# Kernel optimization log

Measured on AMD Instinct MI355X. Metric: run time of the kernel, lower is better.

Reference implementation:

```python
import jax, jax.numpy as jnp
import numpy as np
from jax import lax

MAX_LEN = 40
SOS_ID = 2
VOCAB, EMB, HID, CTX = 32000, 512, 1024, 64
H2 = HID // 2
B, S = 256, 128


def gru_cell(x, h, wih, whh, bih, bhh):
    # PyTorch GRU equations: gates ordered (r, z, n)
    gx = x @ wih.T + bih
    gh = h @ whh.T + bhh
    rx, zx, nx = jnp.split(gx, 3, axis=-1)
    rh, zh, nh = jnp.split(gh, 3, axis=-1)
    r = jax.nn.sigmoid(rx + rh)
    z = jax.nn.sigmoid(zx + zh)
    n = jnp.tanh(nx + r * nh)
    return (1.0 - z) * n + z * h


def setup_inputs() -> dict:
    key = jax.random.key(0)
    ks = jax.random.split(key, 16)
    sd = 0.02
    emb_table = jax.random.normal(ks[0], (VOCAB, EMB), jnp.float32) * sd
    emb_table = emb_table.at[0].set(0.0)  # padding_idx=0
    def w(k, shape):
        return jax.random.normal(k, shape, jnp.float32) * sd
    inp = {
        "input_ids": jax.random.randint(ks[1], (B, S), 0, VOCAB),
        "context_vec": jax.random.normal(ks[2], (B, CTX), jnp.float32),
        "emb_table": emb_table,
        # encoder fwd direction
        "enc_wih_f": w(ks[3], (3 * H2, EMB)),
        "enc_whh_f": w(ks[4], (3 * H2, H2)),
        "enc_bih_f": w(ks[5], (3 * H2,)),
        "enc_bhh_f": w(ks[6], (3 * H2,)),
        # encoder bwd direction
        "enc_wih_b": w(ks[7], (3 * H2, EMB)),
        "enc_whh_b": w(ks[8], (3 * H2, H2)),
        "enc_bih_b": w(ks[9], (3 * H2,)),
        "enc_bhh_b": w(ks[10], (3 * H2,)),
        # decoder GRU: input = emb + hidden + context
        "dec_wih": w(ks[11], (3 * HID, EMB + HID + CTX)),
        "dec_whh": w(ks[12], (3 * HID, HID)),
        "dec_bih": w(ks[13], (3 * HID,)),
        "dec_bhh": w(ks[14], (3 * HID,)),
        "wout": w(ks[15], (VOCAB, HID)),
        "bout": jnp.zeros((VOCAB,), jnp.float32),
    }
    return inp


def reference(input_ids, context_vec, emb_table,
              enc_wih_f, enc_whh_f, enc_bih_f, enc_bhh_f,
              enc_wih_b, enc_whh_b, enc_bih_b, enc_bhh_b,
              dec_wih, dec_whh, dec_bih, dec_bhh, wout, bout):
    b = input_ids.shape[0]
    emb = emb_table[input_ids]                      # [B,S,E]
    emb_t = jnp.swapaxes(emb, 0, 1)                 # [S,B,E]

    def enc_f(h, x):
        return gru_cell(x, h, enc_wih_f, enc_whh_f, enc_bih_f, enc_bhh_f), None

    def enc_b(h, x):
        return gru_cell(x, h, enc_wih_b, enc_whh_b, enc_bih_b, enc_bhh_b), None

    h0 = jnp.zeros((b, H2), emb.dtype)
    hf, _ = lax.scan(enc_f, h0, emb_t)
    hb, _ = lax.scan(enc_b, h0, emb_t[::-1])
    # replicate torch's h_n.view(batch, -1) on a (2,B,H2) tensor (contiguous reshape)
    encoder_ctx = jnp.stack([hf, hb], axis=0).reshape(b, HID)   # [B,HID]

    ctx = jnp.concatenate([encoder_ctx, context_vec], axis=-1)  # [B,HID+CTX]
    h_dec0 = jnp.zeros((b, HID), emb.dtype)
    prev0 = jnp.full((b,), SOS_ID, dtype=jnp.int32)

    def dec_step(carry, _):
        h, prev = carry
        x = jnp.concatenate([emb_table[prev], ctx], axis=-1)
        h = gru_cell(x, h, dec_wih, dec_whh, dec_bih, dec_bhh)
        logits = h @ wout.T + bout                  # [B,V]
        probs = jax.nn.softmax(logits, axis=-1)
        nxt = jnp.argmax(probs, axis=-1).astype(jnp.int32)
        sel = jnp.take_along_axis(probs, nxt[:, None], axis=1)[:, 0]
        lp = jnp.log(sel + 1e-12)
        return (h, nxt), (nxt, lp)

    (_, _), (toks, lps) = lax.scan(dec_step, (h_dec0, prev0), None, length=MAX_LEN)
    return toks.T, lps.T   # [B,MAX_LEN] tokens, [B,MAX_LEN] log-probs
```

## Files before the change

### kernel.cpp

```cpp
#include <hip/hip_runtime.h>
#include <hip/hip_bf16.h>
#include <math.h>

#define B_    256
#define S_    128
#define EMB_  512
#define H2_   512
#define HID_  1024
#define CTX_  64
#define VOC_  32000
#define TMAX_ 40
#define SOS_  2

typedef unsigned short u16;
typedef __attribute__((ext_vector_type(8))) short short8;
typedef __attribute__((ext_vector_type(4))) float f32x4;

__device__ __forceinline__ float4 ld4(const float* p) {
    return *reinterpret_cast<const float4*>(p);
}
__device__ __forceinline__ float sigmoidf_(float x) { return 1.f / (1.f + expf(-x)); }
__device__ __forceinline__ u16 f2bf(float x) {
    union { float f; unsigned int u; } v; v.f = x;
    unsigned int r = v.u + 0x7FFFu + ((v.u >> 16) & 1u);
    return (u16)(r >> 16);
}
__device__ __forceinline__ unsigned pk2(float a, float b) {
    float2 t; t.x = a; t.y = b;
    __hip_bfloat162 h = __float22bfloat162_rn(t);
    return *reinterpret_cast<unsigned*>(&h);
}
__device__ __forceinline__ void merge_top2(float& v1, int& i1, float& v2, int& i2,
                                           float ov1, int oi1, float ov2, int oi2)
{
    if (ov1 > v1 || (ov1 == v1 && oi1 < i1)) {
        float tv = v1; int ti = i1;
        v1 = ov1; i1 = oi1;
        if (ov2 > tv || (ov2 == tv && oi2 < ti)) { v2 = ov2; i2 = oi2; }
        else                                     { v2 = tv;  i2 = ti;  }
    } else {
        if (ov1 > v2 || (ov1 == v2 && oi1 < i2)) { v2 = ov1; i2 = oi1; }
    }
}

template<int BM, int BN, int TM, int TN, int AMODE, int BGATHER, int BIASM>
__launch_bounds__(256)
__global__ void gemm_nt(const float* __restrict__ Ap,
                        const int*   __restrict__ ids,
                        const float* __restrict__ Ex,
                        const float* __restrict__ Bp, int ldb, int bofs,
                        const float* __restrict__ bias,
                        const float* __restrict__ addsrc,
                        float* __restrict__ Cp, int ldc,
                        int lda, int K, int s_base, int sdir)
{
    constexpr int BK = 32;
    __shared__ float As[BK][BM + 4];
    __shared__ float Bs[BK][BN + 4];
    const int t  = threadIdx.x;
    const int tx = t & 15, ty = t >> 4;
    const int m_base = blockIdx.y * BM;
    const int n_base = blockIdx.x * BN;

    float acc[TM][TN];
#pragma unroll
    for (int i = 0; i < TM; ++i)
#pragma unroll
        for (int j = 0; j < TN; ++j) acc[i][j] = 0.f;

    constexpr int A_PER = BM * BK / 4 / 256;
    constexpr int B_PER = BN * BK / 4 / 256;

    for (int k0 = 0; k0 < K; k0 += BK) {
#pragma unroll
        for (int j = 0; j < A_PER; ++j) {
            int f   = t + j * 256;
            int row = f >> 3;
            int kk  = (f & 7) << 2;
            int m   = m_base + row;
            float4 v;
            if constexpr (AMODE == 0) {
                v = ld4(Ap + (size_t)m * lda + k0 + kk);
            } else if constexpr (AMODE == 3) {
                int id = ids[m];
                v = ld4(Ex + (size_t)id * EMB_ + k0 + kk);
            } else {
                int k = k0 + kk;
                if (k < HID_) v = ld4(Ap + (size_t)m * HID_ + k);
                else          v = ld4(Ex + (size_t)m * CTX_ + (k - HID_));
            }
            As[kk + 0][row] = v.x; As[kk + 1][row] = v.y;
            As[kk + 2][row] = v.z; As[kk + 3][row] = v.w;
        }
#pragma unroll
        for (int j = 0; j < B_PER; ++j) {
            int f   = t + j * 256;
            int row = f >> 3;
            int kk  = (f & 7) << 2;
            float4 v;
            if constexpr (BGATHER == 1) {
                int n = n_base + row;
                int s = n >> 8, b = n & 255;
                int id = ids[b * S_ + s_base + sdir * s];
                v = ld4(Ex + (size_t)id * EMB_ + k0 + kk);
            } else {
                v = ld4(Bp + (size_t)(n_base + row) * ldb + bofs + k0 + kk);
            }
            Bs[kk + 0][row] = v.x; Bs[kk + 1][row] = v.y;
            Bs[kk + 2][row] = v.z; Bs[kk + 3][row] = v.w;
        }
        __syncthreads();
#pragma unroll
        for (int kk = 0; kk < BK; ++kk) {
            float a[TM], b[TN];
            *(float4*)&a[0] = ld4(&As[kk][ty * TM]);
            if constexpr (TM == 8) *(float4*)&a[4] = ld4(&As[kk][ty * TM + 4]);
            *(float4*)&b[0] = ld4(&Bs[kk][tx * TN]);
            if constexpr (TN == 8) *(float4*)&b[4] = ld4(&Bs[kk][tx * TN + 4]);
#pragma unroll
            for (int i = 0; i < TM; ++i)
#pragma unroll
                for (int j = 0; j < TN; ++j) acc[i][j] += a[i] * b[j];
        }
        __syncthreads();
    }
#pragma unroll
    for (int i = 0; i < TM; ++i) {
        int m = m_base + ty * TM + i;
#pragma unroll
        for (int j = 0; j < TN; ++j) {
            int n = n_base + tx * TN + j;
            float v = acc[i][j];
            if (bias) v += BIASM ? bias[m] : bias[n];
            if (addsrc) v += addsrc[(size_t)m * ldc + n];
            Cp[(size_t)m * ldc + n] = v;
        }
    }
}

__global__ void whh_trans(const float* __restrict__ whh_f, const float* __restrict__ whh_b,
                          float* __restrict__ whhX_f, float* __restrict__ whhX_b)
{
    int idx = blockIdx.x * 256 + threadIdx.x;
    const float* src = blockIdx.y ? whh_b : whh_f;
    float*       dst = blockIdx.y ? whhX_b : whhX_f;
    int k  = idx / 1536;
    int cc = idx - k * 1536;
    int u  = cc / 3;
    int g  = cc - u * 3;
    dst[idx] = src[(size_t)(g * 512 + u) * 512 + k];
}

#define RECBLK 128

union EncSM {
    struct { float hbuf[2][512][4]; float red[256][25]; } rec;
    struct { float As[32][132]; float Bs[32][132]; } gx;
};

__launch_bounds__(512)
__global__ void enc_fused(const float* __restrict__ grec_f, const float* __restrict__ grec_b,
                          float* __restrict__ gout_f, float* __restrict__ gout_b,
                          const float* __restrict__ whhX_f, const float* __restrict__ whhX_b,
                          const float* __restrict__ bhh_f, const float* __restrict__ bhh_b,
                          const float* __restrict__ wih_f, const float* __restrict__ wih_b,
                          const float* __restrict__ bih_f, const float* __restrict__ bih_b,
                          const int* __restrict__ ids, const float* __restrict__ emb,
                          float* __restrict__ hT, int do_rec, int gx_chunk, int nsteps)
{
    __shared__ __align__(16) EncSM sm;
    const int t = threadIdx.x;

    if (blockIdx.x >= RECBLK) {
        if (gx_chunk < 0) return;
        const int tt  = blockIdx.x - RECBLK;
        const int dz  = tt >= 192;
        const int t192 = dz ? tt - 192 : tt;
        const int m_base = (t192 & 15) * 128;
        const int n_base = (t192 >> 4) * 128;
        const float* W    = dz ? wih_b : wih_f;
        const float* bias = dz ? bih_b : bih_f;
        float*       Cp   = dz ? gout_b : gout_f;
        const int s_base  = dz ? (127 - 8 * gx_chunk) : (8 * gx_chunk);
        const int sdir    = dz ? -1 : 1;
        const int tx = t & 31, ty = t >> 5;

        float acc[8][4];
#pragma unroll
        for (int i = 0; i < 8; ++i)
#pragma unroll
            for (int j = 0; j < 4; ++j) acc[i][j] = 0.f;

        for (int k0 = 0; k0 < 512; k0 += 32) {
#pragma unroll
            for (int j = 0; j < 2; ++j) {
                int f   = t + j * 512;
                int row = f >> 3;
                int kk  = (f & 7) << 2;
                int m   = m_base + row;
                int s   = m >> 8, b = m & 255;
                int id  = ids[b * S_ + s_base + sdir * s];
                float4 v = ld4(emb + (size_t)id * EMB_ + k0 + kk);
                sm.gx.As[kk + 0][row] = v.x; sm.gx.As[kk + 1][row] = v.y;
                sm.gx.As[kk + 2][row] = v.z; sm.gx.As[kk + 3][row] = v.w;
                float4 wv = ld4(W + (size_t)(n_base + row) * 512 + k0 + kk);
                sm.gx.Bs[kk + 0][row] = wv.x; sm.gx.Bs[kk + 1][row] = wv.y;
                sm.gx.Bs[kk + 2][row] = wv.z; sm.gx.Bs[kk + 3][row] = wv.w;
            }
            __syncthreads();
#pragma unroll
            for (int kk = 0; kk < 32; ++kk) {
                float a[8], b[4];
                *(float4*)&a[0] = ld4(&sm.gx.As[kk][ty * 8]);
                *(float4*)&a[4] = ld4(&sm.gx.As[kk][ty * 8 + 4]);
                *(float4*)&b[0] = ld4(&sm.gx.Bs[kk][tx * 4]);
#pragma unroll
                for (int i = 0; i < 8; ++i)
#pragma unroll
                    for (int j = 0; j < 4; ++j) acc[i][j] += a[i] * b[j];
            }
            __syncthreads();
        }
#pragma unroll
        for (int i = 0; i < 8; ++i) {
            int m = m_base + ty * 8 + i;
#pragma unroll
            for (int j = 0; j < 4; ++j) {
                int n = n_base + tx * 4 + j;
                Cp[(size_t)m * 1536 + n] = acc[i][j] + bias[n];
            }
        }
        return;
    }

    if (!do_rec) return;
    const int bid = blockIdx.x;
    const int xcd = bid & 7;
    const int dir = xcd >> 2;
    const int local = (bid >> 3) * 4 + (xcd & 3);
    const int r0 = local * 4;
    const float* gx  = dir ? grec_b : grec_f;
    const float* whx = dir ? whhX_b : whhX_f;
    const float* bhh = dir ? bhh_b : bhh_f;
    float* hTd = hT + (size_t)dir * (256 * 512);

    const int kh = t >> 8;
    const int tu = t & 255;
    const int k_base = kh << 8;

    for (int i = t; i < 2048; i += 512) {
        int r = i >> 9, u = i & 511;
        sm.rec.hbuf[0][u][r] = hTd[(size_t)(r0 + r) * 512 + u];
    }
    float bh[2][3];
#pragma unroll
    for (int uu = 0; uu < 2; ++uu)
#pragma unroll
        for (int g = 0; g < 3; ++g)
            bh[uu][g] = bhh[g * 512 + tu * 2 + uu];
    __syncthreads();

    for (int st = 0; st < nsteps; ++st) {
        const int cur = st & 1, nxt = cur ^ 1;

        float2 gxv[3][4];
        if (!kh) {
#pragma unroll
            for (int g = 0; g < 3; ++g)
#pragma unroll
                for (int r = 0; r < 4; ++r)
                    gxv[g][r] = *(const float2*)&gx[(size_t)((st << 8) + r0 + r) * 1536
                                                    + (g << 9) + (tu << 1)];
        }

        float acc[2][3][4];
#pragma unroll
        for (int uu = 0; uu < 2; ++uu)
#pragma unroll
            for (int g = 0; g < 3; ++g)
#pragma unroll
                for (int r = 0; r < 4; ++r) acc[uu][g][r] = 0.f;

        const float* wp = whx + (size_t)k_base * 1536 + tu * 6;
#pragma unroll 4
        for (int kk = 0; kk < 256; ++kk) {
            float4 hv = *(const float4*)&sm.rec.hbuf[cur][k_base + kk][0];
            float2 w0 = *(const float2*)(wp + 0);
            float2 w1 = *(const float2*)(wp + 2);
            float2 w2 = *(const float2*)(wp + 4);
            const float* hvp = (const float*)&hv;
#pragma unroll
            for (int r = 0; r < 4; ++r) {
                float h = hvp[r];
                acc[0][0][r] += w0.x * h;
                acc[0][1][r] += w0.y * h;
                acc[0][2][r] += w1.x * h;
                acc[1][0][r] += w1.y * h;
                acc[1][1][r] += w2.x * h;
                acc[1][2][r] += w2.y * h;
            }
            wp += 1536;
        }

        if (kh) {
#pragma unroll
            for (int uu = 0; uu < 2; ++uu)
#pragma unroll
                for (int g = 0; g < 3; ++g)
#pragma unroll
                    for (int r = 0; r < 4; ++r)
                        sm.rec.red[tu][(uu * 3 + g) * 4 + r] = acc[uu][g][r];
        }
        __syncthreads();
        if (!kh) {
#pragma unroll
            for (int uu = 0; uu < 2; ++uu)
#pragma unroll
                for (int g = 0; g < 3; ++g)
#pragma unroll
                    for (int r = 0; r < 4; ++r)
                        acc[uu][g][r] += sm.rec.red[tu][(uu * 3 + g) * 4 + r];
#pragma unroll
            for (int uu = 0; uu < 2; ++uu) {
                int u = tu * 2 + uu;
#pragma unroll
                for (int r = 0; r < 4; ++r) {
                    float gr = uu ? gxv[0][r].y : gxv[0][r].x;
                    float gz = uu ? gxv[1][r].y : gxv[1][r].x;
                    float gn = uu ? gxv[2][r].y : gxv[2][r].x;
                    float hold = sm.rec.hbuf[cur][u][r];
                    float rg = sigmoidf_(gr + acc[uu][0][r] + bh[uu][0]);
                    float zg = sigmoidf_(gz + acc[uu][1][r] + bh[uu][1]);
                    float ng = tanhf(gn + rg * (acc[uu][2][r] + bh[uu][2]));
                    sm.rec.hbuf[nxt][u][r] = (1.f - zg) * ng + zg * hold;
                }
            }
        }
        __syncthreads();
    }

    const int lb = nsteps & 1;
    for (int i = t; i < 2048; i += 512) {
        int r = i >> 9, u = i & 511;
        hTd[(size_t)(r0 + r) * 512 + u] = sm.rec.hbuf[lb][u][r];
    }
}

__global__ void zerof(float* __restrict__ p, int n)
{
    int i = blockIdx.x * 256 + threadIdx.x;
    if (i < n) p[i] = 0.f;
}

__global__ void init_dec(float* __restrict__ hdec, u16* __restrict__ hbf, int* __restrict__ prev)
{
    int i = blockIdx.x * 256 + threadIdx.x;
    hdec[i] = 0.f; hbf[i] = 0;
    if (i < B_) prev[i] = SOS_;
}

__global__ void hcat_build(const float* __restrict__ hT, float* __restrict__ hcat)
{
    int idx = blockIdx.x * 256 + threadIdx.x;
    int b = idx >> 10, k = idx & 1023;
    int d = b >> 7;
    int rr = ((2 * b) & 255) + (k >> 9);
    int kk = k & 511;
    hcat[idx] = hT[(size_t)d * 131072 + (size_t)rr * 512 + kk];
}

__launch_bounds__(256)
__global__ void dec_gemm2(const float* __restrict__ hdec, const int* __restrict__ prev,
                          const float* __restrict__ emb,
                          const float* __restrict__ dwhh, const float* __restrict__ dwih,
                          const float* __restrict__ dbhh, const float* __restrict__ gctx,
                          float* __restrict__ ghbuf, float* __restrict__ gibuf)
{
    constexpr int BK = 32;
    __shared__ float As[BK][68];
    __shared__ float Bs[BK][68];
    const int t  = threadIdx.x;
    const int tx = t & 15, ty = t >> 4;
    const bool isH = blockIdx.y < 4;
    const int m_base = (isH ? blockIdx.y : (blockIdx.y - 4)) * 64;
    const int n_base = blockIdx.x * 64;
    const int K   = isH ? 1024 : 512;
    const float* Bp = isH ? dwhh : dwih;
    const int ldb  = isH ? 1024 : 1600;
    float* Cp = isH ? ghbuf : gibuf;

    float acc[4][4];
#pragma unroll
    for (int i = 0; i < 4; ++i)
#pragma unroll
        for (int j = 0; j < 4; ++j) acc[i][j] = 0.f;

    for (int k0 = 0; k0 < K; k0 += BK) {
#pragma unroll
        for (int j = 0; j < 2; ++j) {
            int f   = t + j * 256;
            int row = f >> 3;
            int kk  = (f & 7) << 2;
            int m   = m_base + row;
            float4 v;
            if (isH) v = ld4(hdec + (size_t)m * HID_ + k0 + kk);
            else     v = ld4(emb + (size_t)prev[m] * EMB_ + k0 + kk);
            As[kk + 0][row] = v.x; As[kk + 1][row] = v.y;
            As[kk + 2][row] = v.z; As[kk + 3][row] = v.w;
            float4 w = ld4(Bp + (size_t)(n_base + row) * ldb + k0 + kk);
            Bs[kk + 0][row] = w.x; Bs[kk + 1][row] = w.y;
            Bs[kk + 2][row] = w.z; Bs[kk + 3][row] = w.w;
        }
        __syncthreads();
#pragma unroll
        for (int kk = 0; kk < BK; ++kk) {
            float a[4], b[4];
            *(float4*)&a[0] = ld4(&As[kk][ty * 4]);
            *(float4*)&b[0] = ld4(&Bs[kk][tx * 4]);
#pragma unroll
            for (int i = 0; i < 4; ++i)
#pragma unroll
                for (int j = 0; j < 4; ++j) acc[i][j] += a[i] * b[j];
        }
        __syncthreads();
    }
#pragma unroll
    for (int i = 0; i < 4; ++i) {
        int m = m_base + ty * 4 + i;
#pragma unroll
        for (int j = 0; j < 4; ++j) {
            int n = n_base + tx * 4 + j;
            float v = acc[i][j];
            if (isH) v += dbhh[n];
            else     v += gctx[(size_t)m * 3072 + n];
            Cp[(size_t)m * 3072 + n] = v;
        }
    }
}

__global__ void dec_combine(const float* __restrict__ gi, const float* __restrict__ gh,
                            float* __restrict__ hdec, u16* __restrict__ hbf)
{
    int idx = blockIdx.x * 256 + threadIdx.x;
    int b = idx >> 10, u = idx & 1023;
    size_t gb = (size_t)b * 3072;
    float r = sigmoidf_(gi[gb + u]            + gh[gb + u]);
    float z = sigmoidf_(gi[gb + HID_ + u]     + gh[gb + HID_ + u]);
    float n = tanhf    (gi[gb + 2 * HID_ + u] + r * gh[gb + 2 * HID_ + u]);
    float v = (1.f - z) * n + z * hdec[idx];
    hdec[idx] = v;
    hbf[idx] = f2bf(v);
}

__launch_bounds__(512)
__global__ void gemm_logits(const u16* __restrict__ A, const float* __restrict__ Wf,
                            const float* __restrict__ bias,
                            float* __restrict__ pmax, float* __restrict__ psum,
                            float* __restrict__ ptv, int* __restrict__ pti)
{
    __shared__ u16 As[256][72];
    __shared__ u16 Bs[128][72];
    const int t = threadIdx.x;
    const int lane = t & 63, wave = t >> 6;
    const int wm = (wave & 3) * 64, wn = (wave >> 2) * 64;
    const int n0 = blockIdx.x * 128;
    f32x4 acc[4][4];
#pragma unroll
    for (int i = 0; i < 4; ++i)
#pragma unroll
        for (int j = 0; j < 4; ++j) acc[i][j] = (f32x4){0.f, 0.f, 0.f, 0.f};
    const int arow = t >> 1, aoff = (t & 1) * 32;
    const int brow = t >> 2, boff = (t & 3) * 16;

    for (int k0 = 0; k0 < 1024; k0 += 64) {
#pragma unroll
        for (int q = 0; q < 4; ++q) {
            *(uint4*)&As[arow][aoff + q * 8] =
                *(const uint4*)(A + (size_t)arow * 1024 + k0 + aoff + q * 8);
        }
        const float* wr = Wf + (size_t)(n0 + brow) * 1024 + k0 + boff;
#pragma unroll
        for (int q = 0; q < 2; ++q) {
            float4 x = ld4(wr + q * 8);
            float4 y = ld4(wr + q * 8 + 4);
            uint4 o;
            o.x = pk2(x.x, x.y); o.y = pk2(x.z, x.w);
            o.z = pk2(y.x, y.y); o.w = pk2(y.z, y.w);
            *(uint4*)&Bs[brow][boff + q * 8] = o;
        }
        __syncthreads();
#pragma unroll
        for (int s = 0; s < 2; ++s) {
            short8 a[4], b[4];
            int j0 = s * 32 + (lane >> 4) * 8;
#pragma unroll
            for (int i = 0; i < 4; ++i) {
                a[i] = *(const short8*)&As[wm + i * 16 + (lane & 15)][j0];
                b[i] = *(const short8*)&Bs[wn + i * 16 + (lane & 15)][j0];
            }
#pragma unroll
            for (int i = 0; i < 4; ++i)
#pragma unroll
                for (int j = 0; j < 4; ++j)
                    acc[i][j] = __builtin_amdgcn_mfma_f32_16x16x32_bf16(a[i], b[j], acc[i][j], 0, 0, 0);
        }
        __syncthreads();
    }

    const int htile = blockIdx.x * 2 + (wn >> 6);
    float bn[4]; int jx[4];
#pragma unroll
    for (int j = 0; j < 4; ++j) { jx[j] = n0 + wn + j * 16 + (lane & 15); bn[j] = bias[jx[j]]; }
#pragma unroll
    for (int i = 0; i < 4; ++i) {
#pragma unroll
        for (int rr = 0; rr < 4; ++rr) {
            float v[4];
#pragma unroll
            for (int j = 0; j < 4; ++j) v[j] = acc[i][j][rr] + bn[j];
            float v1 = v[0], v2 = -3.4e38f; int i1 = jx[0], i2 = 0x7fffffff;
#pragma unroll
            for (int j = 1; j < 4; ++j) {
                if (v[j] > v1)      { v2 = v1; i2 = i1; v1 = v[j]; i1 = jx[j]; }
                else if (v[j] > v2) { v2 = v[j]; i2 = jx[j]; }
            }
#pragma unroll
            for (int mask = 1; mask <= 8; mask <<= 1) {
                float ov1 = __shfl_xor(v1, mask), ov2 = __shfl_xor(v2, mask);
                int   oi1 = __shfl_xor(i1, mask), oi2 = __shfl_xor(i2, mask);
                merge_top2(v1, i1, v2, i2, ov1, oi1, ov2, oi2);
            }
            float rmax = v1;
            float s = 0.f;
#pragma unroll
            for (int j = 0; j < 4; ++j) s += expf(v[j] - rmax);
#pragma unroll
            for (int mask = 1; mask <= 8; mask <<= 1) s += __shfl_xor(s, mask);
            if ((lane & 15) == 0) {
                int row = wm + i * 16 + (lane >> 4) * 4 + rr;
                size_t base = (size_t)row * 500 + htile;
                pmax[base] = rmax; psum[base] = s;
                ptv[base * 2] = v1; ptv[base * 2 + 1] = v2;
                pti[base * 2] = i1; pti[base * 2 + 1] = i2;
            }
        }
    }
}

__launch_bounds__(256)
__global__ void dec_reduce(const float* __restrict__ pmax, const float* __restrict__ psum,
                           const float* __restrict__ ptv, const int* __restrict__ pti,
                           const float* __restrict__ hdec, const float* __restrict__ wout,
                           const float* __restrict__ bout,
                           float* __restrict__ out, int* __restrict__ prev, int tstep)
{
    __shared__ float sv[256]; __shared__ int sti[256]; __shared__ int ssl[256];
    __shared__ float cvv[1000]; __shared__ int cii[1000];
    __shared__ float c8v[8]; __shared__ int c8i[8]; __shared__ float c8e[8];
    const int b = blockIdx.x, tid = threadIdx.x;
    const float* pm = pmax + (size_t)b * 500;
    const float* ps = psum + (size_t)b * 500;

    float m = -3.4e38f;
    for (int i = tid; i < 500; i += 256) m = fmaxf(m, pm[i]);
    sv[tid] = m; __syncthreads();
    for (int off = 128; off; off >>= 1) { if (tid < off) sv[tid] = fmaxf(sv[tid], sv[tid + off]); __syncthreads(); }
    float gmax = sv[0]; __syncthreads();

    float s = 0.f;
    for (int i = tid; i < 500; i += 256) s += ps[i] * expf(pm[i] - gmax);
    sv[tid] = s; __syncthreads();
    for (int off = 128; off; off >>= 1) { if (tid < off) sv[tid] += sv[tid + off]; __syncthreads(); }
    float gsum = sv[0]; __syncthreads();

    for (int i = tid; i < 1000; i += 256) { cvv[i] = ptv[(size_t)b * 1000 + i]; cii[i] = pti[(size_t)b * 1000 + i]; }
    __syncthreads();

    for (int c = 0; c < 8; ++c) {
        float bv = -3.4e38f; int bi = 0x7fffffff, bs = 0;
        for (int i = tid; i < 1000; i += 256) {
            float v = cvv[i]; int ix = cii[i];
            if (v > bv || (v == bv && ix < bi)) { bv = v; bi = ix; bs = i; }
        }
        sv[tid] = bv; sti[tid] = bi; ssl[tid] = bs; __syncthreads();
        for (int off = 128; off; off >>= 1) {
            if (tid < off) {
                if (sv[tid + off] > sv[tid] ||
                    (sv[tid + off] == sv[tid] && sti[tid + off] < sti[tid])) {
                    sv[tid] = sv[tid + off]; sti[tid] = sti[tid + off]; ssl[tid] = ssl[tid + off];
                }
            }
            __syncthreads();
        }
        if (tid == 0) { c8v[c] = sv[0]; c8i[c] = sti[0]; cvv[ssl[0]] = -3.4e38f; }
        __syncthreads();
    }

    {
        int lane = tid & 63, wv = tid >> 6;
        const float* hr = hdec + (size_t)b * HID_;
        for (int c = wv; c < 8; c += 4) {
            const float* wr = wout + (size_t)c8i[c] * HID_;
            float a = 0.f;
            for (int k = lane * 4; k < HID_; k += 256) {
                float4 x = ld4(hr + k), y = ld4(wr + k);
                a += x.x * y.x + x.y * y.y + x.z * y.z + x.w * y.w;
            }
#pragma unroll
            for (int off = 32; off; off >>= 1) a += __shfl_down(a, off);
            if (lane == 0) c8e[c] = a + bout[c8i[c]];
        }
    }
    __syncthreads();

    if (tid == 0) {
        float bv = c8e[0]; int bi = c8i[0]; float av = c8v[0];
        for (int c = 1; c < 8; ++c)
            if (c8e[c] > bv || (c8e[c] == bv && c8i[c] < bi)) { bv = c8e[c]; bi = c8i[c]; av = c8v[c]; }
        float p = expf(av - gmax) / gsum;
        float lp = logf(p + 1e-12f);
        out[(size_t)b * TMAX_ + tstep] = (float)bi;
        out[B_ * TMAX_ + (size_t)b * TMAX_ + tstep] = lp;
        prev[b] = bi;
    }
}

extern "C" void kernel_launch(void* const* d_in, const int* in_sizes, int n_in,
                              void* d_out, int out_size, void* d_ws, size_t ws_size,
                              hipStream_t stream)
{
    const int*   ids   = (const int*)  d_in[0];
    const float* cvec  = (const float*)d_in[1];
    const float* emb   = (const float*)d_in[2];
    const float* wih_f = (const float*)d_in[3];
    const float* whh_f = (const float*)d_in[4];
    const float* bih_f = (const float*)d_in[5];
    const float* bhh_f = (const float*)d_in[6];
    const float* wih_b = (const float*)d_in[7];
    const float* whh_b = (const float*)d_in[8];
    const float* bih_b = (const float*)d_in[9];
    const float* bhh_b = (const float*)d_in[10];
    const float* dwih  = (const float*)d_in[11];
    const float* dwhh  = (const float*)d_in[12];
    const float* dbih  = (const float*)d_in[13];
    const float* dbhh  = (const float*)d_in[14];
    const float* wout  = (const float*)d_in[15];
    const float* bout  = (const float*)d_in[16];
    float* out = (float*)d_out;

    float* w      = (float*)d_ws;
    float* buf0_f = w;
    float* buf0_b = w + 3145728;
    float* buf1_f = w + 6291456;
    float* buf1_b = w + 9437184;
    float* hT     = w + 12582912;
    float* hcat   = w + 12845056;
    float* hdec   = w + 13107200;
    float* gctx   = w + 13369344;
    u16*   hdecb  = (u16*)(w + 14155776);
    int*   prev   = (int*)(w + 14286848);
    float* whhX_f = w + 14287104;
    float* whhX_b = w + 15073536;
    float* gibuf  = buf0_f;
    float* ghbuf  = buf0_f + 786432;
    float* pmax   = buf0_f + 1572864;
    float* psum   = buf0_f + 1700864;
    float* ptv    = buf0_f + 1828864;
    int*   pti    = (int*)(buf0_f + 2084864);

    zerof<<<1024, 256, 0, stream>>>(hT, 262144);
    init_dec<<<1024, 256, 0, stream>>>(hdec, hdecb, prev);
    whh_trans<<<dim3(3072, 2), 256, 0, stream>>>(whh_f, whh_b, whhX_f, whhX_b);

    enc_fused<<<512, 512, 0, stream>>>(
        buf0_f, buf0_b, buf0_f, buf0_b, whhX_f, whhX_b, bhh_f, bhh_b,
        wih_f, wih_b, bih_f, bih_b, ids, emb, hT, 0, 0, 8);
    for (int c = 1; c < 16; ++c) {
        float* rf = ((c - 1) & 1) ? buf1_f : buf0_f;
        float* rb = ((c - 1) & 1) ? buf1_b : buf0_b;
        float* of = (c & 1) ? buf1_f : buf0_f;
        float* ob = (c & 1) ? buf1_b : buf0_b;
        enc_fused<<<512, 512, 0, stream>>>(
            rf, rb, of, ob, whhX_f, whhX_b, bhh_f, bhh_b,
            wih_f, wih_b, bih_f, bih_b, ids, emb, hT, 1, c, 8);
    }
    enc_fused<<<512, 512, 0, stream>>>(
        buf1_f, buf1_b, buf1_f, buf1_b, whhX_f, whhX_b, bhh_f, bhh_b,
        wih_f, wih_b, bih_f, bih_b, ids, emb, hT, 1, -1, 8);

    hcat_build<<<1024, 256, 0, stream>>>(hT, hcat);

    gemm_nt<64, 64, 4, 4, 2, 0, 0><<<dim3(48, 4), 256, 0, stream>>>(
        hcat, nullptr, cvec, dwih, 1600, 512, dbih, nullptr,
        gctx, 3072, 1024, 1088, 0, 0);

    for (int t = 0; t < TMAX_; ++t) {
        dec_gemm2<<<dim3(48, 8), 256, 0, stream>>>(
            hdec, prev, emb, dwhh, dwih, dbhh, gctx, ghbuf, gibuf);
        dec_combine<<<1024, 256, 0, stream>>>(gibuf, ghbuf, hdec, hdecb);
        gemm_logits<<<dim3(250, 1), 512, 0, stream>>>(hdecb, wout, bout,
                                                      pmax, psum, ptv, pti);
        dec_reduce<<<256, 256, 0, stream>>>(pmax, psum, ptv, pti,
                                            hdec, wout, bout, out, prev, t);
    }
}
```

Before: 10.65 ms.

## Pre-convert output weights to bf16 and restructure encoder recurrence to one unit per thread

The encoder recurrent weights are now laid out gate-major (k, gate, unit), and each of the 512 threads computes one hidden unit over the full K=512. This removes the split-K shared-memory reduction and one barrier per step, at the cost of a longer serial dot product per thread. Separately, the 32000x1024 output projection is converted to bf16 once, so the per-step logits GEMM loads half the bytes and skips the repeated fp32-to-bf16 packing. That path is used only when the workspace is large enough, which adds one conversion kernel and about 64MB of scratch.

```diff
diff --git a/kernel.cpp b/kernel.cpp
--- a/kernel.cpp
+++ b/kernel.cpp
@@ -139,29 +139,36 @@
 }
 
 __global__ void whh_trans(const float* __restrict__ whh_f, const float* __restrict__ whh_b,
-                          float* __restrict__ whhX_f, float* __restrict__ whhX_b)
+                          float* __restrict__ whhU_f, float* __restrict__ whhU_b)
 {
     int idx = blockIdx.x * 256 + threadIdx.x;
     const float* src = blockIdx.y ? whh_b : whh_f;
-    float*       dst = blockIdx.y ? whhX_b : whhX_f;
+    float*       dst = blockIdx.y ? whhU_b : whhU_f;
     int k  = idx / 1536;
-    int cc = idx - k * 1536;
-    int u  = cc / 3;
-    int g  = cc - u * 3;
+    int rem = idx - k * 1536;
+    int g  = rem >> 9;
+    int u  = rem & 511;
     dst[idx] = src[(size_t)(g * 512 + u) * 512 + k];
 }
 
+__global__ void wbf_conv(const float* __restrict__ wout, unsigned* __restrict__ wbf)
+{
+    int idx = blockIdx.x * 256 + threadIdx.x;
+    float2 v = *reinterpret_cast<const float2*>(wout + (size_t)idx * 2);
+    wbf[idx] = pk2(v.x, v.y);
+}
+
 #define RECBLK 128
 
 union EncSM {
-    struct { float hbuf[2][512][4]; float red[256][25]; } rec;
+    struct { float hbuf[2][512][4]; } rec;
     struct { float As[32][132]; float Bs[32][132]; } gx;
 };
 
 __launch_bounds__(512)
 __global__ void enc_fused(const float* __restrict__ grec_f, const float* __restrict__ grec_b,
                           float* __restrict__ gout_f, float* __restrict__ gout_b,
-                          const float* __restrict__ whhX_f, const float* __restrict__ whhX_b,
+                          const float* __restrict__ whhU_f, const float* __restrict__ whhU_b,
                           const float* __restrict__ bhh_f, const float* __restrict__ bhh_b,
                           const float* __restrict__ wih_f, const float* __restrict__ wih_b,
                           const float* __restrict__ bih_f, const float* __restrict__ bih_b,
@@ -240,110 +247,63 @@
     const int local = (bid >> 3) * 4 + (xcd & 3);
     const int r0 = local * 4;
     const float* gx  = dir ? grec_b : grec_f;
-    const float* whx = dir ? whhX_b : whhX_f;
+    const float* whx = dir ? whhU_b : whhU_f;
     const float* bhh = dir ? bhh_b : bhh_f;
     float* hTd = hT + (size_t)dir * (256 * 512);
 
-    const int kh = t >> 8;
-    const int tu = t & 255;
-    const int k_base = kh << 8;
-
-    for (int i = t; i < 2048; i += 512) {
-        int r = i >> 9, u = i & 511;
+    const int u = t;
+
+#pragma unroll
+    for (int r = 0; r < 4; ++r)
         sm.rec.hbuf[0][u][r] = hTd[(size_t)(r0 + r) * 512 + u];
-    }
-    float bh[2][3];
-#pragma unroll
-    for (int uu = 0; uu < 2; ++uu)
-#pragma unroll
-        for (int g = 0; g < 3; ++g)
-            bh[uu][g] = bhh[g * 512 + tu * 2 + uu];
+    const float bh0 = bhh[u], bh1 = bhh[512 + u], bh2 = bhh[1024 + u];
     __syncthreads();
 
     for (int st = 0; st < nsteps; ++st) {
         const int cur = st & 1, nxt = cur ^ 1;
 
-        float2 gxv[3][4];
-        if (!kh) {
-#pragma unroll
-            for (int g = 0; g < 3; ++g)
-#pragma unroll
-                for (int r = 0; r < 4; ++r)
-                    gxv[g][r] = *(const float2*)&gx[(size_t)((st << 8) + r0 + r) * 1536
-                                                    + (g << 9) + (tu << 1)];
-        }
-
-        float acc[2][3][4];
-#pragma unroll
-        for (int uu = 0; uu < 2; ++uu)
-#pragma unroll
-            for (int g = 0; g < 3; ++g)
-#pragma unroll
-                for (int r = 0; r < 4; ++r) acc[uu][g][r] = 0.f;
-
-        const float* wp = whx + (size_t)k_base * 1536 + tu * 6;
-#pragma unroll 4
-        for (int kk = 0; kk < 256; ++kk) {
-            float4 hv = *(const float4*)&sm.rec.hbuf[cur][k_base + kk][0];
-            float2 w0 = *(const float2*)(wp + 0);
-            float2 w1 = *(const float2*)(wp + 2);
-            float2 w2 = *(const float2*)(wp + 4);
+        float gx0[4], gx1[4], gx2[4];
+#pragma unroll
+        for (int r = 0; r < 4; ++r) {
+            size_t base = (size_t)((st << 8) + r0 + r) * 1536 + u;
+            gx0[r] = gx[base];
+            gx1[r] = gx[base + 512];
+            gx2[r] = gx[base + 1024];
+        }
+
+        float acc0[4] = {0.f,0.f,0.f,0.f};
+        float acc1[4] = {0.f,0.f,0.f,0.f};
+        float acc2[4] = {0.f,0.f,0.f,0.f};
+        const float* wp = whx + u;
+#pragma unroll 8
+        for (int kk = 0; kk < 512; ++kk) {
+            float4 hv = *(const float4*)&sm.rec.hbuf[cur][kk][0];
+            float w0 = wp[0], w1 = wp[512], w2 = wp[1024];
             const float* hvp = (const float*)&hv;
 #pragma unroll
             for (int r = 0; r < 4; ++r) {
-                float h = hvp[r];
-                acc[0][0][r] += w0.x * h;
-                acc[0][1][r] += w0.y * h;
-                acc[0][2][r] += w1.x * h;
-                acc[1][0][r] += w1.y * h;
-                acc[1][1][r] += w2.x * h;
-                acc[1][2][r] += w2.y * h;
+                acc0[r] += w0 * hvp[r];
+                acc1[r] += w1 * hvp[r];
+                acc2[r] += w2 * hvp[r];
             }
             wp += 1536;
         }
 
-        if (kh) {
-#pragma unroll
-            for (int uu = 0; uu < 2; ++uu)
-#pragma unroll
-                for (int g = 0; g < 3; ++g)
-#pragma unroll
-                    for (int r = 0; r < 4; ++r)
-                        sm.rec.red[tu][(uu * 3 + g) * 4 + r] = acc[uu][g][r];
-        }
-        __syncthreads();
-        if (!kh) {
-#pragma unroll
-            for (int uu = 0; uu < 2; ++uu)
-#pragma unroll
-                for (int g = 0; g < 3; ++g)
-#pragma unroll
-                    for (int r = 0; r < 4; ++r)
-                        acc[uu][g][r] += sm.rec.red[tu][(uu * 3 + g) * 4 + r];
-#pragma unroll
-            for (int uu = 0; uu < 2; ++uu) {
-                int u = tu * 2 + uu;
-#pragma unroll
-                for (int r = 0; r < 4; ++r) {
-                    float gr = uu ? gxv[0][r].y : gxv[0][r].x;
-                    float gz = uu ? gxv[1][r].y : gxv[1][r].x;
-                    float gn = uu ? gxv[2][r].y : gxv[2][r].x;
-                    float hold = sm.rec.hbuf[cur][u][r];
-                    float rg = sigmoidf_(gr + acc[uu][0][r] + bh[uu][0]);
-                    float zg = sigmoidf_(gz + acc[uu][1][r] + bh[uu][1]);
-                    float ng = tanhf(gn + rg * (acc[uu][2][r] + bh[uu][2]));
-                    sm.rec.hbuf[nxt][u][r] = (1.f - zg) * ng + zg * hold;
-                }
-            }
+#pragma unroll
+        for (int r = 0; r < 4; ++r) {
+            float hold = sm.rec.hbuf[cur][u][r];
+            float rg = sigmoidf_(gx0[r] + acc0[r] + bh0);
+            float zg = sigmoidf_(gx1[r] + acc1[r] + bh1);
+            float ng = tanhf(gx2[r] + rg * (acc2[r] + bh2));
+            sm.rec.hbuf[nxt][u][r] = (1.f - zg) * ng + zg * hold;
         }
         __syncthreads();
     }
 
     const int lb = nsteps & 1;
-    for (int i = t; i < 2048; i += 512) {
-        int r = i >> 9, u = i & 511;
+#pragma unroll
+    for (int r = 0; r < 4; ++r)
         hTd[(size_t)(r0 + r) * 512 + u] = sm.rec.hbuf[lb][u][r];
-    }
 }
 
 __global__ void zerof(float* __restrict__ p, int n)
@@ -454,6 +414,7 @@
 
 __launch_bounds__(512)
 __global__ void gemm_logits(const u16* __restrict__ A, const float* __restrict__ Wf,
+                            const u16* __restrict__ Wbf,
                             const float* __restrict__ bias,
                             float* __restrict__ pmax, float* __restrict__ psum,
                             float* __restrict__ ptv, int* __restrict__ pti)
@@ -478,15 +439,21 @@
             *(uint4*)&As[arow][aoff + q * 8] =
                 *(const uint4*)(A + (size_t)arow * 1024 + k0 + aoff + q * 8);
         }
-        const float* wr = Wf + (size_t)(n0 + brow) * 1024 + k0 + boff;
-#pragma unroll
-        for (int q = 0; q < 2; ++q) {
-            float4 x = ld4(wr + q * 8);
-            float4 y = ld4(wr + q * 8 + 4);
-            uint4 o;
-            o.x = pk2(x.x, x.y); o.y = pk2(x.z, x.w);
-            o.z = pk2(y.x, y.y); o.w = pk2(y.z, y.w);
-            *(uint4*)&Bs[brow][boff + q * 8] = o;
+        if (Wbf) {
+            const u16* wr = Wbf + (size_t)(n0 + brow) * 1024 + k0 + boff;
+            *(uint4*)&Bs[brow][boff]     = *(const uint4*)(wr);
+            *(uint4*)&Bs[brow][boff + 8] = *(const uint4*)(wr + 8);
+        } else {
+            const float* wr = Wf + (size_t)(n0 + brow) * 1024 + k0 + boff;
+#pragma unroll
+            for (int q = 0; q < 2; ++q) {
+                float4 x = ld4(wr + q * 8);
+                float4 y = ld4(wr + q * 8 + 4);
+                uint4 o;
+                o.x = pk2(x.x, x.y); o.y = pk2(x.z, x.w);
+                o.z = pk2(y.x, y.y); o.w = pk2(y.z, y.w);
+                *(uint4*)&Bs[brow][boff + q * 8] = o;
+            }
         }
         __syncthreads();
 #pragma unroll
@@ -659,8 +626,10 @@
     float* gctx   = w + 13369344;
     u16*   hdecb  = (u16*)(w + 14155776);
     int*   prev   = (int*)(w + 14286848);
-    float* whhX_f = w + 14287104;
-    float* whhX_b = w + 15073536;
+    float* whhU_f = w + 14287104;
+    float* whhU_b = w + 15073536;
+    u16*   wbf    = (u16*)(w + 15859968);
+    const int use_wbf = (ws_size >= (size_t)(15859968 + 16384000) * 4);
     float* gibuf  = buf0_f;
     float* ghbuf  = buf0_f + 786432;
     float* pmax   = buf0_f + 1572864;
@@ -670,10 +639,10 @@
 
     zerof<<<1024, 256, 0, stream>>>(hT, 262144);
     init_dec<<<1024, 256, 0, stream>>>(hdec, hdecb, prev);
-    whh_trans<<<dim3(3072, 2), 256, 0, stream>>>(whh_f, whh_b, whhX_f, whhX_b);
+    whh_trans<<<dim3(3072, 2), 256, 0, stream>>>(whh_f, whh_b, whhU_f, whhU_b);
 
     enc_fused<<<512, 512, 0, stream>>>(
-        buf0_f, buf0_b, buf0_f, buf0_b, whhX_f, whhX_b, bhh_f, bhh_b,
+        buf0_f, buf0_b, buf0_f, buf0_b, whhU_f, whhU_b, bhh_f, bhh_b,
         wih_f, wih_b, bih_f, bih_b, ids, emb, hT, 0, 0, 8);
     for (int c = 1; c < 16; ++c) {
         float* rf = ((c - 1) & 1) ? buf1_f : buf0_f;
@@ -681,14 +650,17 @@
         float* of = (c & 1) ? buf1_f : buf0_f;
         float* ob = (c & 1) ? buf1_b : buf0_b;
         enc_fused<<<512, 512, 0, stream>>>(
-            rf, rb, of, ob, whhX_f, whhX_b, bhh_f, bhh_b,
+            rf, rb, of, ob, whhU_f, whhU_b, bhh_f, bhh_b,
             wih_f, wih_b, bih_f, bih_b, ids, emb, hT, 1, c, 8);
     }
     enc_fused<<<512, 512, 0, stream>>>(
-        buf1_f, buf1_b, buf1_f, buf1_b, whhX_f, whhX_b, bhh_f, bhh_b,
+        buf1_f, buf1_b, buf1_f, buf1_b, whhU_f, whhU_b, bhh_f, bhh_b,
         wih_f, wih_b, bih_f, bih_b, ids, emb, hT, 1, -1, 8);
 
     hcat_build<<<1024, 256, 0, stream>>>(hT, hcat);
+
+    if (use_wbf)
+        wbf_conv<<<64000, 256, 0, stream>>>(wout, (unsigned*)wbf);
 
     gemm_nt<64, 64, 4, 4, 2, 0, 0><<<dim3(48, 4), 256, 0, stream>>>(
         hcat, nullptr, cvec, dwih, 1600, 512, dbih, nullptr,
@@ -698,8 +670,9 @@
         dec_gemm2<<<dim3(48, 8), 256, 0, stream>>>(
             hdec, prev, emb, dwhh, dwih, dbhh, gctx, ghbuf, gibuf);
         dec_combine<<<1024, 256, 0, stream>>>(gibuf, ghbuf, hdec, hdecb);
-        gemm_logits<<<dim3(250, 1), 512, 0, stream>>>(hdecb, wout, bout,
-                                                      pmax, psum, ptv, pti);
+        gemm_logits<<<dim3(250, 1), 512, 0, stream>>>(
+            hdecb, wout, use_wbf ? wbf : (const u16*)nullptr, bout,
+            pmax, psum, ptv, pti);
         dec_reduce<<<256, 256, 0, stream>>>(pmax, psum, ptv, pti,
                                             hdec, wout, bout, out, prev, t);
     }
```

Measured after the change: 10.26 ms. 3.6% less time.
